# Kernel optimization log

Measured on AMD Instinct MI355X. Metric: run time of the kernel, lower is better.

The kernel has to match this reference:

```python
import jax, jax.numpy as jnp
import numpy as np

FILTERS = 64
HIDDEN = 128
T_PRED = 24
DILATIONS = (1, 2, 4, 8, 16, 32)
N_DIL = len(DILATIONS)
FEAT = 15
B = 1024
L_ENC = 168


def setup_inputs() -> dict:
    key = jax.random.key(0)
    ks = jax.random.split(key, 16)
    s = 0.05
    d_in = 1 + FEAT  # prev_output (1) concat current feature
    inp = {
        "decoder_features": jax.random.normal(ks[0], (B, T_PRED, FEAT), jnp.float32),
        "decoder_init_input": jax.random.normal(ks[1], (B, 1), jnp.float32),
        "encoder_states": jax.random.normal(ks[2], (N_DIL, B, L_ENC, FILTERS), jnp.float32),
        # dense_1: d_in -> filters (tanh)
        "W1": jax.random.normal(ks[3], (d_in, FILTERS), jnp.float32) * s,
        "b1": jnp.zeros((FILTERS,), jnp.float32),
        # dense_2: filters -> 2*filters (bias)
        "W2": jax.random.normal(ks[4], (FILTERS, 2 * FILTERS), jnp.float32) * s,
        "b2": jnp.zeros((2 * FILTERS,), jnp.float32),
        # dense_3: filters -> 2*filters (no bias)
        "W3": jax.random.normal(ks[5], (FILTERS, 2 * FILTERS), jnp.float32) * s,
        # dense_4: filters -> 2*filters (bias)
        "W4": jax.random.normal(ks[6], (FILTERS, 2 * FILTERS), jnp.float32) * s,
        "b4": jnp.zeros((2 * FILTERS,), jnp.float32),
        # dense_5: n_dil*filters -> hidden (relu)
        "W5": jax.random.normal(ks[7], (N_DIL * FILTERS, HIDDEN), jnp.float32) * s,
        "b5": jnp.zeros((HIDDEN,), jnp.float32),
        # dense_6: hidden -> 1
        "W6": jax.random.normal(ks[8], (HIDDEN, 1), jnp.float32) * s,
        "b6": jnp.zeros((1,), jnp.float32),
    }
    return inp


def _decode(decoder_features, decoder_init_input, encoder_states,
            W1, b1, W2, b2, W3, W4, b4, W5, b5, W6, b6):
    L = encoder_states.shape[2]
    # 'appended' holds the inputs written back into each dilation's state
    # (the growing-concat part of encoder_states in the original loop).
    appended0 = jnp.zeros((N_DIL, decoder_features.shape[0], T_PRED, FILTERS),
                          dtype=decoder_features.dtype)

    def step(carry, t):
        prev, appended = carry
        cur = jnp.concatenate([prev, decoder_features[:, t, :]], axis=1)  # [B, 1+FEAT]
        inputs = jnp.tanh(cur @ W1 + b1)  # [B, F]
        skips_list = []
        for i, d in enumerate(DILATIONS):
            # grown-state read index is (L + t) - d; if t >= d it lands in the
            # appended region (step t-d), otherwise in the original encoder state.
            idx_app = jnp.clip(t - d, 0, T_PRED - 1)
            idx_orig = jnp.clip(L + t - d, 0, L - 1)
            st_app = jax.lax.dynamic_index_in_dim(appended[i], idx_app, axis=1, keepdims=False)
            st_orig = jax.lax.dynamic_index_in_dim(encoder_states[i], idx_orig, axis=1, keepdims=False)
            state = jnp.where(t >= d, st_app, st_orig)  # [B, F]
            dilated = state @ W2 + b2 + inputs @ W3  # [B, 2F]
            conv_filter, conv_gate = dilated[:, :FILTERS], dilated[:, FILTERS:]
            gated = jnp.tanh(conv_filter) * jax.nn.sigmoid(conv_gate)
            out = gated @ W4 + b4  # [B, 2F]
            skips, residuals = out[:, :FILTERS], out[:, FILTERS:]
            inputs = inputs + residuals
            appended = appended.at[i, :, t, :].set(inputs)
            skips_list.append(skips)
        skip = jax.nn.relu(jnp.concatenate(skips_list, axis=1))  # [B, N_DIL*F]
        h = jax.nn.relu(skip @ W5 + b5)
        y = h @ W6 + b6  # [B, 1]
        return (y, appended), y

    (_, _), ys = jax.lax.scan(step, (decoder_init_input, appended0),
                              jnp.arange(T_PRED))
    return jnp.transpose(ys, (1, 0, 2))  # [B, T, 1]


def reference(decoder_features, decoder_init_input, encoder_states,
              W1, b1, W2, b2, W3, W4, b4, W5, b5, W6, b6):
    return _decode(decoder_features, decoder_init_input, encoder_states,
                   W1, b1, W2, b2, W3, W4, b4, W5, b5, W6, b6)
```

## Files before the change

kernel.cpp:

```cpp
#include <hip/hip_runtime.h>

typedef _Float16 h16;
typedef _Float16 half4 __attribute__((ext_vector_type(4)));
typedef _Float16 half8 __attribute__((ext_vector_type(8)));
typedef float floatx4 __attribute__((ext_vector_type(4)));

#define B_TOT 1024
#define T_STEPS 24
#define F 64
#define C2 128
#define FEAT 15
#define L_ENC 168
#define HID 128
#define R 16
#define BLK 256
#define FP 72

__device__ __forceinline__ floatx4 mfma16(half8 a, half8 b, floatx4 c) {
  return __builtin_amdgcn_mfma_f32_16x16x32_f16(a, b, c, 0, 0, 0);
}

#define BAR() asm volatile("s_waitcnt lgkmcnt(0)\n\ts_barrier" ::: "memory")

#define PIN(x) asm volatile("" : "+v"(x))

__device__ __forceinline__ float tanh_fast(float x) {
  float cx = fminf(fmaxf(x, -15.f), 15.f);
  float e  = __builtin_amdgcn_exp2f(-2.885390081777927f * cx);
  return (1.f - e) * __builtin_amdgcn_rcpf(1.f + e);
}
__device__ __forceinline__ float gate_fast(float f, float g) {
  float cf = fminf(fmaxf(f, -15.f), 15.f);
  float cg = fminf(fmaxf(g, -30.f), 30.f);
  float ef = __builtin_amdgcn_exp2f(-2.885390081777927f * cf);
  float eg = __builtin_amdgcn_exp2f(-1.4426950408889634f * cg);
  return (1.f - ef) * __builtin_amdgcn_rcpf((1.f + ef) * (1.f + eg));
}

__global__ void prep_w5(const float* __restrict__ gW5, h16* __restrict__ wsW5) {
  int t = blockIdx.x * 256 + threadIdx.x;
  if (t >= 12 * 8 * 64) return;
  int lane = t & 63, nt = (t >> 6) & 7, ktg = t >> 9;
  int n  = nt * 16 + (lane & 15);
  int kb = ktg * 32 + (lane >> 4) * 8;
  half8 v;
  #pragma unroll
  for (int j = 0; j < 8; ++j) v[j] = (h16)gW5[(size_t)(kb + j) * C2 + n];
  *(half8*)&wsW5[(size_t)t * 8] = v;
}

__global__ __launch_bounds__(BLK, 1) void decoder_v10(
    const float* __restrict__ dec_feat,
    const float* __restrict__ dec_init,
    const float* __restrict__ enc,
    const float* __restrict__ gW1, const float* __restrict__ gb1,
    const float* __restrict__ gW2, const float* __restrict__ gb2,
    const float* __restrict__ gW3,
    const float* __restrict__ gW4, const float* __restrict__ gb4,
    const h16*  __restrict__ wsW5, const float* __restrict__ gb5,
    const float* __restrict__ gW6, const float* __restrict__ gb6,
    float* __restrict__ out)
{
  __shared__ alignas(16) h16 ringL[31][R][FP];
  __shared__ alignas(16) h16 enc5L[T_STEPS][R][FP];
  __shared__ alignas(16) h16 xH[R][FP];
  __shared__ alignas(16) h16 gatedH[R][FP];
  __shared__ alignas(16) h16 skipH[R][FP];
  __shared__ alignas(16) h16 featH[T_STEPS][R][16];
  __shared__ alignas(16) float ypartS[R][4];

  const int tid  = threadIdx.x;
  const int w    = tid >> 6;
  const int lane = tid & 63;
  const int m16  = lane & 15;
  const int q    = lane >> 4;
  const int q8   = q * 8;
  const int b0   = blockIdx.x * R;
  const int col4 = w * 16 + q * 4;

  half8 rW1;
  #pragma unroll
  for (int j = 0; j < 8; ++j) {
    int k = q8 + j;
    rW1[j] = (k < 16) ? (h16)gW1[k * F + (w * 16 + m16)] : (h16)0.0f;
  }
  half8 rW2[2][2], rW3[2][2], rW4[2][2];
  #pragma unroll
  for (int h = 0; h < 2; ++h) {
    int n = (w + 4 * h) * 16 + m16;
    #pragma unroll
    for (int kt = 0; kt < 2; ++kt) {
      half8 v2, v3, v4;
      #pragma unroll
      for (int j = 0; j < 8; ++j) {
        int k = kt * 32 + q8 + j;
        v2[j] = (h16)gW2[k * C2 + n];
        v3[j] = (h16)gW3[k * C2 + n];
        v4[j] = (h16)gW4[k * C2 + n];
      }
      rW2[h][kt] = v2; rW3[h][kt] = v3; rW4[h][kt] = v4;
    }
  }
  half8 w5r[6][4];
  #pragma unroll
  for (int i = 0; i < 6; ++i)
    #pragma unroll
    for (int kt = 0; kt < 2; ++kt)
      #pragma unroll
      for (int nn = 0; nn < 2; ++nn)
        w5r[i][kt * 2 + nn] =
            *(const half8*)&wsW5[(size_t)((((2 * i + kt) * 8) + (w + 4 * nn)) * 64 + lane) * 8];

  floatx4 rb1v  = *(const floatx4*)&gb1[col4];
  floatx4 rb2fv = *(const floatx4*)&gb2[col4];
  floatx4 rb2gv = *(const floatx4*)&gb2[64 + col4];
  floatx4 rb4sv = *(const floatx4*)&gb4[col4];
  floatx4 rb4rv = *(const floatx4*)&gb4[64 + col4];
  floatx4 rb5av = *(const floatx4*)&gb5[col4];
  floatx4 rb5bv = *(const floatx4*)&gb5[64 + col4];
  floatx4 rw6av = *(const floatx4*)&gW6[col4];
  floatx4 rw6bv = *(const floatx4*)&gW6[64 + col4];
  const float rb6   = gb6[0];
  const float rInit = dec_init[b0 + m16];

  {
    int mm = tid >> 4, kk = (tid & 15) * 4;
    #pragma unroll 1
    for (int it = 0; it < 55; ++it) {
      int i, s; h16* dst;
      if (it < 31) {
        i = (it >= 15) ? 4 : (it >= 7) ? 3 : (it >= 3) ? 2 : (it >= 1) ? 1 : 0;
        s = it - ((1 << i) - 1);
        dst = &ringL[it][mm][kk];
      } else { i = 5; s = it - 31; dst = &enc5L[s][mm][kk]; }
      int d = 1 << i;
      const float* sp = enc + (((size_t)i * B_TOT + b0 + mm) * L_ENC + (L_ENC + s - d)) * F + kk;
      float4 v = *(const float4*)sp;
      half4 hv; hv[0] = (h16)v.x; hv[1] = (h16)v.y; hv[2] = (h16)v.z; hv[3] = (h16)v.w;
      *(half4*)dst = hv;
    }
  }
  for (int p = tid; p < T_STEPS * R; p += BLK) {
    int tt = p >> 4, row = p & 15;
    const float* sp = dec_feat + (size_t)(b0 + row) * (T_STEPS * FEAT) + tt * FEAT;
    half8 v0, v1;
    v0[0] = (h16)0.0f;
    #pragma unroll
    for (int j = 0; j < 7; ++j) v0[1 + j] = (h16)sp[j];
    #pragma unroll
    for (int j = 0; j < 8; ++j) v1[j] = (h16)sp[7 + j];
    *(half8*)&featH[tt][row][0] = v0;
    *(half8*)&featH[tt][row][8] = v1;
  }
  __syncthreads();

  auto loadStat = [&](half8* dst, int i, int t) {
    const h16* p;
    if (i == 5) p = &enc5L[t][m16][0];
    else {
      const int d = 1 << i;
      p = &ringL[((1 << i) - 1) + (t & (d - 1))][m16][0];
    }
    dst[0] = *(const half8*)(p + q8);
    dst[1] = *(const half8*)(p + 32 + q8);
  };

  float xr[4];

  for (int t = 0; t < T_STEPS; ++t) {
    PIN(rW1);
    #pragma unroll
    for (int h = 0; h < 2; ++h)
      #pragma unroll
      for (int kt = 0; kt < 2; ++kt) { PIN(rW2[h][kt]); PIN(rW3[h][kt]); PIN(rW4[h][kt]); }
    #pragma unroll
    for (int i = 0; i < 6; ++i)
      #pragma unroll
      for (int k = 0; k < 4; ++k) PIN(w5r[i][k]);
    PIN(rb1v); PIN(rb2fv); PIN(rb2gv); PIN(rb4sv); PIN(rb4rv);
    PIN(rb5av); PIN(rb5bv); PIN(rw6av); PIN(rw6bv);

    float yv;
    if (t == 0) yv = rInit;
    else {
      float4 yp = *(const float4*)&ypartS[m16][0];
      yv = (yp.x + yp.y + yp.z + yp.w) + rb6;
    }
    if (t > 0 && w == 0 && q == 0)
      out[(size_t)(b0 + m16) * T_STEPS + (t - 1)] = yv;

    half8 bCur;
    if (q < 2) {
      bCur = *(const half8*)&featH[t][m16][q8];
    } else {
      #pragma unroll
      for (int j = 0; j < 8; ++j) bCur[j] = (h16)0.0f;
    }
    if (q == 0) bCur[0] = (h16)yv;
    floatx4 accX = {0.f, 0.f, 0.f, 0.f};
    accX = mfma16(rW1, bCur, accX);
    half8 stat[2];
    loadStat(stat, 0, t);
    half4 xv;
    #pragma unroll
    for (int j = 0; j < 4; ++j) {
      float v = tanh_fast(accX[j] + rb1v[j]);
      xr[j] = v;
      xv[j] = (h16)v;
    }
    *(half4*)&xH[m16][col4] = xv;
    BAR();

    floatx4 hAccA = {0.f, 0.f, 0.f, 0.f};
    floatx4 hAccB = {0.f, 0.f, 0.f, 0.f};

    #pragma unroll
    for (int i = 0; i < 6; ++i) {
      const int d = 1 << i;
      half8 xB0 = *(const half8*)&xH[m16][q8];
      half8 xB1 = *(const half8*)&xH[m16][32 + q8];
      half8 stN[2];
      if (i < 5) loadStat(stN, i + 1, t);

      floatx4 aF0 = {0.f,0.f,0.f,0.f}, aF1 = {0.f,0.f,0.f,0.f};
      floatx4 aG0 = {0.f,0.f,0.f,0.f}, aG1 = {0.f,0.f,0.f,0.f};
      aF0 = mfma16(rW2[0][0], stat[0], aF0);
      aF1 = mfma16(rW2[0][1], stat[1], aF1);
      aG0 = mfma16(rW2[1][0], stat[0], aG0);
      aG1 = mfma16(rW2[1][1], stat[1], aG1);
      aF0 = mfma16(rW3[0][0], xB0, aF0);
      aF1 = mfma16(rW3[0][1], xB1, aF1);
      aG0 = mfma16(rW3[1][0], xB0, aG0);
      aG1 = mfma16(rW3[1][1], xB1, aG1);
      half4 gv;
      #pragma unroll
      for (int j = 0; j < 4; ++j) {
        float f = aF0[j] + aF1[j] + rb2fv[j];
        float g = aG0[j] + aG1[j] + rb2gv[j];
        gv[j] = (h16)gate_fast(f, g);
      }
      *(half4*)&gatedH[m16][col4] = gv;
      BAR();

      half8 gB0 = *(const half8*)&gatedH[m16][q8];
      half8 gB1 = *(const half8*)&gatedH[m16][32 + q8];
      floatx4 oS0 = {0.f,0.f,0.f,0.f}, oS1 = {0.f,0.f,0.f,0.f};
      floatx4 oR0 = {0.f,0.f,0.f,0.f}, oR1 = {0.f,0.f,0.f,0.f};
      oS0 = mfma16(rW4[0][0], gB0, oS0);
      oS1 = mfma16(rW4[0][1], gB1, oS1);
      oR0 = mfma16(rW4[1][0], gB0, oR0);
      oR1 = mfma16(rW4[1][1], gB1, oR1);
      half4 sv, xv2;
      #pragma unroll
      for (int j = 0; j < 4; ++j) {
        float s = oS0[j] + oS1[j] + rb4sv[j];
        sv[j] = (h16)fmaxf(s, 0.0f);
        float xn = xr[j] + (oR0[j] + oR1[j] + rb4rv[j]);
        xr[j] = xn;
        xv2[j] = (h16)xn;
      }
      *(half4*)&skipH[m16][col4] = sv;
      *(half4*)&xH[m16][col4]   = xv2;
      if (i < 5) *(half4*)&ringL[((1 << i) - 1) + (t & (d - 1))][m16][col4] = xv2;
      BAR();

      half8 sB0 = *(const half8*)&skipH[m16][q8];
      half8 sB1 = *(const half8*)&skipH[m16][32 + q8];
      hAccA = mfma16(w5r[i][0], sB0, hAccA);
      hAccA = mfma16(w5r[i][2], sB1, hAccA);
      hAccB = mfma16(w5r[i][1], sB0, hAccB);
      hAccB = mfma16(w5r[i][3], sB1, hAccB);

      if (i < 5) { stat[0] = stN[0]; stat[1] = stN[1]; }
    }

    {
      float vv = 0.f;
      #pragma unroll
      for (int j = 0; j < 4; ++j) {
        vv += fmaxf(hAccA[j] + rb5av[j], 0.0f) * rw6av[j];
        vv += fmaxf(hAccB[j] + rb5bv[j], 0.0f) * rw6bv[j];
      }
      vv += __shfl_xor(vv, 16);
      vv += __shfl_xor(vv, 32);
      if (q == 0) ypartS[m16][w] = vv;
    }
    BAR();
  }

  {
    float4 yp = *(const float4*)&ypartS[m16][0];
    float yv = (yp.x + yp.y + yp.z + yp.w) + rb6;
    if (w == 0 && q == 0)
      out[(size_t)(b0 + m16) * T_STEPS + (T_STEPS - 1)] = yv;
  }
}

extern "C" void kernel_launch(void* const* d_in, const int* in_sizes, int n_in,
                              void* d_out, int out_size, void* d_ws, size_t ws_size,
                              hipStream_t stream) {
  const float* dec_feat = (const float*)d_in[0];
  const float* dec_init = (const float*)d_in[1];
  const float* enc      = (const float*)d_in[2];
  const float* W1 = (const float*)d_in[3];
  const float* b1 = (const float*)d_in[4];
  const float* W2 = (const float*)d_in[5];
  const float* b2 = (const float*)d_in[6];
  const float* W3 = (const float*)d_in[7];
  const float* W4 = (const float*)d_in[8];
  const float* b4 = (const float*)d_in[9];
  const float* W5 = (const float*)d_in[10];
  const float* b5 = (const float*)d_in[11];
  const float* W6 = (const float*)d_in[12];
  const float* b6 = (const float*)d_in[13];
  float* out = (float*)d_out;
  h16* wsW5 = (h16*)d_ws;

  prep_w5<<<24, 256, 0, stream>>>(W5, wsW5);
  decoder_v10<<<dim3(B_TOT / R), dim3(BLK), 0, stream>>>(
      dec_feat, dec_init, enc, W1, b1, W2, b2, W3, W4, b4, wsW5, b5, W6, b6, out);
}
```

Measured before the change: 440.7 us.

## Precompute feature projection in prep kernel and compute input tanh per lane

The feature part of the dense_1 projection (features times W1 plus bias) now runs in a separate parallel prep kernel that writes to workspace. The decoder keeps only the rank-1 term from the previous output, so each lane computes the tanh for the input columns it needs directly. This removes the per-step MFMA, the LDS store and the barrier before the dilation loop. Next-step feature values are prefetched from global memory. The PIN register pinning and the upper clamps in the tanh and gate helpers are also removed, and the time loop is no longer unrolled. In exchange there is an extra kernel launch and the feature data is read through global memory.

```diff
diff --git a/kernel.cpp b/kernel.cpp
--- a/kernel.cpp
+++ b/kernel.cpp
@@ -11,29 +11,26 @@
 #define C2 128
 #define FEAT 15
 #define L_ENC 168
-#define HID 128
 #define R 16
 #define BLK 256
 #define FP 72
 
+#define WS_XF_BYTE 98304
+
 __device__ __forceinline__ floatx4 mfma16(half8 a, half8 b, floatx4 c) {
   return __builtin_amdgcn_mfma_f32_16x16x32_f16(a, b, c, 0, 0, 0);
 }
 
 #define BAR() asm volatile("s_waitcnt lgkmcnt(0)\n\ts_barrier" ::: "memory")
 
-#define PIN(x) asm volatile("" : "+v"(x))
-
 __device__ __forceinline__ float tanh_fast(float x) {
-  float cx = fminf(fmaxf(x, -15.f), 15.f);
+  float cx = fmaxf(x, -30.f);
   float e  = __builtin_amdgcn_exp2f(-2.885390081777927f * cx);
   return (1.f - e) * __builtin_amdgcn_rcpf(1.f + e);
 }
 __device__ __forceinline__ float gate_fast(float f, float g) {
-  float cf = fminf(fmaxf(f, -15.f), 15.f);
-  float cg = fminf(fmaxf(g, -30.f), 30.f);
-  float ef = __builtin_amdgcn_exp2f(-2.885390081777927f * cf);
-  float eg = __builtin_amdgcn_exp2f(-1.4426950408889634f * cg);
+  float ef = __builtin_amdgcn_exp2f(-2.885390081777927f * fmaxf(f, -30.f));
+  float eg = __builtin_amdgcn_exp2f(-1.4426950408889634f * fmaxf(g, -80.f));
   return (1.f - ef) * __builtin_amdgcn_rcpf((1.f + ef) * (1.f + eg));
 }
 
@@ -49,15 +46,38 @@
   *(half8*)&wsW5[(size_t)t * 8] = v;
 }
 
-__global__ __launch_bounds__(BLK, 1) void decoder_v10(
-    const float* __restrict__ dec_feat,
+__global__ void prep_xfeat(const float* __restrict__ df, const float* __restrict__ W1,
+                           const float* __restrict__ b1, float* __restrict__ xf) {
+  int idx = blockIdx.x * 256 + threadIdx.x;
+  if (idx >= B_TOT * T_STEPS * 16) return;
+  int c4 = (idx & 15) * 4;
+  int bt = idx >> 4;
+  int b  = bt / T_STEPS, t = bt - b * T_STEPS;
+  const float* fp = df + (size_t)b * (T_STEPS * FEAT) + t * FEAT;
+  float acc[4];
+  #pragma unroll
+  for (int j = 0; j < 4; ++j) acc[j] = b1[c4 + j];
+  #pragma unroll
+  for (int f = 0; f < FEAT; ++f) {
+    float fv = (float)(h16)fp[f];
+    #pragma unroll
+    for (int j = 0; j < 4; ++j)
+      acc[j] += fv * (float)(h16)W1[(1 + f) * F + c4 + j];
+  }
+  float* op = xf + ((size_t)b * T_STEPS + t) * F + c4;
+  #pragma unroll
+  for (int j = 0; j < 4; ++j) op[j] = acc[j];
+}
+
+__global__ __launch_bounds__(BLK, 1) void decoder_v13(
     const float* __restrict__ dec_init,
     const float* __restrict__ enc,
-    const float* __restrict__ gW1, const float* __restrict__ gb1,
+    const float* __restrict__ gW1,
     const float* __restrict__ gW2, const float* __restrict__ gb2,
     const float* __restrict__ gW3,
     const float* __restrict__ gW4, const float* __restrict__ gb4,
-    const h16*  __restrict__ wsW5, const float* __restrict__ gb5,
+    const h16*  __restrict__ wsW5, const float* __restrict__ xFeat,
+    const float* __restrict__ gb5,
     const float* __restrict__ gW6, const float* __restrict__ gb6,
     float* __restrict__ out)
 {
@@ -66,7 +86,6 @@
   __shared__ alignas(16) h16 xH[R][FP];
   __shared__ alignas(16) h16 gatedH[R][FP];
   __shared__ alignas(16) h16 skipH[R][FP];
-  __shared__ alignas(16) h16 featH[T_STEPS][R][16];
   __shared__ alignas(16) float ypartS[R][4];
 
   const int tid  = threadIdx.x;
@@ -78,12 +97,6 @@
   const int b0   = blockIdx.x * R;
   const int col4 = w * 16 + q * 4;
 
-  half8 rW1;
-  #pragma unroll
-  for (int j = 0; j < 8; ++j) {
-    int k = q8 + j;
-    rW1[j] = (k < 16) ? (h16)gW1[k * F + (w * 16 + m16)] : (h16)0.0f;
-  }
   half8 rW2[2][2], rW3[2][2], rW4[2][2];
   #pragma unroll
   for (int h = 0; h < 2; ++h) {
@@ -111,7 +124,12 @@
         w5r[i][kt * 2 + nn] =
             *(const half8*)&wsW5[(size_t)((((2 * i + kt) * 8) + (w + 4 * nn)) * 64 + lane) * 8];
 
-  floatx4 rb1v  = *(const floatx4*)&gb1[col4];
+  half8 w1h0, w1h1; half4 w1h4;
+  #pragma unroll
+  for (int j = 0; j < 8; ++j) { w1h0[j] = (h16)gW1[q8 + j]; w1h1[j] = (h16)gW1[32 + q8 + j]; }
+  #pragma unroll
+  for (int j = 0; j < 4; ++j) w1h4[j] = (h16)gW1[col4 + j];
+
   floatx4 rb2fv = *(const floatx4*)&gb2[col4];
   floatx4 rb2gv = *(const floatx4*)&gb2[64 + col4];
   floatx4 rb4sv = *(const floatx4*)&gb4[col4];
@@ -140,46 +158,24 @@
       *(half4*)dst = hv;
     }
   }
-  for (int p = tid; p < T_STEPS * R; p += BLK) {
-    int tt = p >> 4, row = p & 15;
-    const float* sp = dec_feat + (size_t)(b0 + row) * (T_STEPS * FEAT) + tt * FEAT;
-    half8 v0, v1;
-    v0[0] = (h16)0.0f;
-    #pragma unroll
-    for (int j = 0; j < 7; ++j) v0[1 + j] = (h16)sp[j];
-    #pragma unroll
-    for (int j = 0; j < 8; ++j) v1[j] = (h16)sp[7 + j];
-    *(half8*)&featH[tt][row][0] = v0;
-    *(half8*)&featH[tt][row][8] = v1;
-  }
+  const float* xfb = xFeat + (size_t)(b0 + m16) * T_STEPS * F;
+  float4 xf0, xf1, xf2, xf3, xf4;
+  xf0 = *(const float4*)(xfb + q8);      xf1 = *(const float4*)(xfb + q8 + 4);
+  xf2 = *(const float4*)(xfb + 32 + q8); xf3 = *(const float4*)(xfb + 32 + q8 + 4);
+  xf4 = *(const float4*)(xfb + col4);
   __syncthreads();
 
   auto loadStat = [&](half8* dst, int i, int t) {
-    const h16* p;
-    if (i == 5) p = &enc5L[t][m16][0];
-    else {
-      const int d = 1 << i;
-      p = &ringL[((1 << i) - 1) + (t & (d - 1))][m16][0];
-    }
+    const h16* p = (i == 5) ? &enc5L[t][m16][0]
+                            : &ringL[((1 << i) - 1) + (t & ((1 << i) - 1))][m16][0];
     dst[0] = *(const half8*)(p + q8);
     dst[1] = *(const half8*)(p + 32 + q8);
   };
 
   float xr[4];
 
+  #pragma unroll 1
   for (int t = 0; t < T_STEPS; ++t) {
-    PIN(rW1);
-    #pragma unroll
-    for (int h = 0; h < 2; ++h)
-      #pragma unroll
-      for (int kt = 0; kt < 2; ++kt) { PIN(rW2[h][kt]); PIN(rW3[h][kt]); PIN(rW4[h][kt]); }
-    #pragma unroll
-    for (int i = 0; i < 6; ++i)
-      #pragma unroll
-      for (int k = 0; k < 4; ++k) PIN(w5r[i][k]);
-    PIN(rb1v); PIN(rb2fv); PIN(rb2gv); PIN(rb4sv); PIN(rb4rv);
-    PIN(rb5av); PIN(rb5bv); PIN(rw6av); PIN(rw6bv);
-
     float yv;
     if (t == 0) yv = rInit;
     else {
@@ -188,28 +184,29 @@
     }
     if (t > 0 && w == 0 && q == 0)
       out[(size_t)(b0 + m16) * T_STEPS + (t - 1)] = yv;
-
-    half8 bCur;
-    if (q < 2) {
-      bCur = *(const half8*)&featH[t][m16][q8];
-    } else {
-      #pragma unroll
-      for (int j = 0; j < 8; ++j) bCur[j] = (h16)0.0f;
-    }
-    if (q == 0) bCur[0] = (h16)yv;
-    floatx4 accX = {0.f, 0.f, 0.f, 0.f};
-    accX = mfma16(rW1, bCur, accX);
+    const float yh = (float)(h16)yv;
+
+    half8 xB0, xB1;
+    #pragma unroll
+    for (int j = 0; j < 4; ++j) {
+      xB0[j]     = (h16)tanh_fast(xf0[j] + (float)w1h0[j] * yh);
+      xB0[4 + j] = (h16)tanh_fast(xf1[j] + (float)w1h0[4 + j] * yh);
+      xB1[j]     = (h16)tanh_fast(xf2[j] + (float)w1h1[j] * yh);
+      xB1[4 + j] = (h16)tanh_fast(xf3[j] + (float)w1h1[4 + j] * yh);
+    }
+    #pragma unroll
+    for (int j = 0; j < 4; ++j)
+      xr[j] = tanh_fast(xf4[j] + (float)w1h4[j] * yh);
+
+    if (t + 1 < T_STEPS) {
+      const float* xfn = xfb + (t + 1) * F;
+      xf0 = *(const float4*)(xfn + q8);      xf1 = *(const float4*)(xfn + q8 + 4);
+      xf2 = *(const float4*)(xfn + 32 + q8); xf3 = *(const float4*)(xfn + 32 + q8 + 4);
+      xf4 = *(const float4*)(xfn + col4);
+    }
+
     half8 stat[2];
     loadStat(stat, 0, t);
-    half4 xv;
-    #pragma unroll
-    for (int j = 0; j < 4; ++j) {
-      float v = tanh_fast(accX[j] + rb1v[j]);
-      xr[j] = v;
-      xv[j] = (h16)v;
-    }
-    *(half4*)&xH[m16][col4] = xv;
-    BAR();
 
     floatx4 hAccA = {0.f, 0.f, 0.f, 0.f};
     floatx4 hAccB = {0.f, 0.f, 0.f, 0.f};
@@ -217,8 +214,10 @@
     #pragma unroll
     for (int i = 0; i < 6; ++i) {
       const int d = 1 << i;
-      half8 xB0 = *(const half8*)&xH[m16][q8];
-      half8 xB1 = *(const half8*)&xH[m16][32 + q8];
+      if (i > 0) {
+        xB0 = *(const half8*)&xH[m16][q8];
+        xB1 = *(const half8*)&xH[m16][32 + q8];
+      }
       half8 stN[2];
       if (i < 5) loadStat(stN, i + 1, t);
 
@@ -314,9 +313,11 @@
   const float* W6 = (const float*)d_in[12];
   const float* b6 = (const float*)d_in[13];
   float* out = (float*)d_out;
-  h16* wsW5 = (h16*)d_ws;
+  h16*   wsW5 = (h16*)d_ws;
+  float* wsXF = (float*)((char*)d_ws + WS_XF_BYTE);
 
   prep_w5<<<24, 256, 0, stream>>>(W5, wsW5);
-  decoder_v10<<<dim3(B_TOT / R), dim3(BLK), 0, stream>>>(
-      dec_feat, dec_init, enc, W1, b1, W2, b2, W3, W4, b4, wsW5, b5, W6, b6, out);
-}
+  prep_xfeat<<<1536, 256, 0, stream>>>(dec_feat, W1, b1, wsXF);
+  decoder_v13<<<dim3(B_TOT / R), dim3(BLK), 0, stream>>>(
+      dec_init, enc, W1, W2, b2, W3, W4, b4, wsW5, wsXF, b5, W6, b6, out);
+}
```

Measured after the change: 452.1 us. 1.03x slower.
